# Kernel tuning notes

Measured on AMD Instinct MI355X. Metric: run time of the kernel, lower is better.

The kernel has to match this reference:

```python
import jax, jax.numpy as jnp
import numpy as np

B, H, L, D = 8, 16, 1024, 64

def setup_inputs() -> dict:
    key = jax.random.key(0)
    kq, kk, kv = jax.random.split(key, 3)
    q = jax.random.normal(kq, (B, H, L, D), dtype=jnp.float32)
    k = jax.random.normal(kk, (B, H, L, D), dtype=jnp.float32)
    v = jax.random.normal(kv, (B, H, L, D), dtype=jnp.float32)
    # causal mask, broadcast over batch and head
    mask = jnp.tril(jnp.ones((L, L), dtype=jnp.int32))[None, None, :, :]
    return {"q": q, "k": k, "v": v, "mask": mask}

def reference(q, k, v, mask):
    b, h, l, d = q.shape
    # FAITHFUL to original: k.view(b, h, d, l) is a reshape, NOT a transpose
    k_t = k.reshape(b, h, d, l)
    score = jnp.matmul(q, k_t) / np.sqrt(d).astype(np.float32)  # [b,h,l,l]
    # FAITHFUL to original bug: masked_fill(mask==0, -e) with e=1e-12
    score = jnp.where(mask == 0, jnp.float32(-1e-12), score)
    attn = jax.nn.softmax(score, axis=-1)
    out = jnp.matmul(attn, v)  # [b,h,l,d]
    return (out, attn)
```

## Files before the change

kernel.cpp:

```cpp
#include <hip/hip_runtime.h>

#define L_  1024
#define D_  64
#define TM  128
#define TN  64
#define LDK 72
#define NT  (L_ / TN)

typedef __attribute__((ext_vector_type(8))) short          short8;
typedef __attribute__((ext_vector_type(8))) unsigned short ushort8;
typedef __attribute__((ext_vector_type(4))) float          f32x4;

__device__ __forceinline__ unsigned short bf16r(float f) {
    unsigned u = __builtin_bit_cast(unsigned, f);
    u += 0x7fffu + ((u >> 16) & 1u);
    return (unsigned short)(u >> 16);
}

__global__ __launch_bounds__(256, 2)
void sdpa_kernel(const float* __restrict__ q, const float* __restrict__ kmat,
                 const float* __restrict__ v, float* __restrict__ out,
                 float* __restrict__ attn)
{
    __shared__ __align__(16) unsigned short Qs[TM * LDK];
    __shared__ __align__(16) unsigned short Ks[TN * LDK];
    __shared__ __align__(16) unsigned short Vs[D_ * LDK];
    __shared__ __align__(16) unsigned short Ps[TM * LDK];

    const int t    = threadIdx.x;
    const int wave = t >> 6;
    const int lane = t & 63;
    const int quad = lane >> 4;
    const int l15  = lane & 15;
    const int rt   = blockIdx.x;
    const int bh   = blockIdx.y;
    const int m0   = rt * TM;
    const int rowA = wave * 32;

    const float* qb = q    + (size_t)bh * (L_ * D_);
    const float* kb = kmat + (size_t)bh * (L_ * D_);
    const float* vb = v    + (size_t)bh * (L_ * D_);
    float* outb  = out  + (size_t)bh * (L_ * D_);
    float* attnb = attn + (size_t)bh * ((size_t)L_ * L_);

    #pragma unroll
    for (int i = 0; i < 8; ++i) {
        int idx = (i * 256 + t) * 4;
        int m = idx >> 6, c = idx & 63;
        float4 f = *(const float4*)&qb[(size_t)(m0 + m) * D_ + c];
        ushort4 b;
        b.x = bf16r(f.x); b.y = bf16r(f.y); b.z = bf16r(f.z); b.w = bf16r(f.w);
        *(ushort4*)&Qs[m * LDK + c] = b;
    }

    auto stageK = [&](int nt) {
        const int ng = t & 31, kg = t >> 5;
        const float* src = kb + (size_t)(kg * 8) * L_ + nt * TN + 2 * ng;
        float2 a[8];
        #pragma unroll
        for (int j = 0; j < 8; ++j) a[j] = *(const float2*)(src + (size_t)j * L_);
        ushort8 r0, r1;
        #pragma unroll
        for (int j = 0; j < 8; ++j) { r0[j] = bf16r(a[j].x); r1[j] = bf16r(a[j].y); }
        *(ushort8*)&Ks[(2 * ng)     * LDK + kg * 8] = r0;
        *(ushort8*)&Ks[(2 * ng + 1) * LDK + kg * 8] = r1;
    };
    auto stageV = [&](int nt) {
        const int cg = t & 31, ngp = t >> 5;
        const float* src = vb + (size_t)(nt * TN + ngp * 8) * D_ + 2 * cg;
        float2 a[8];
        #pragma unroll
        for (int j = 0; j < 8; ++j) a[j] = *(const float2*)(src + (size_t)j * D_);
        ushort8 r0, r1;
        #pragma unroll
        for (int j = 0; j < 8; ++j) { r0[j] = bf16r(a[j].x); r1[j] = bf16r(a[j].y); }
        *(ushort8*)&Vs[(2 * cg)     * LDK + ngp * 8] = r0;
        *(ushort8*)&Vs[(2 * cg + 1) * LDK + ngp * 8] = r1;
    };

    auto computeScore = [&](f32x4 (&acc)[2][4]) {
        #pragma unroll
        for (int ks = 0; ks < 2; ++ks) {
            short8 af[2];
            #pragma unroll
            for (int tr = 0; tr < 2; ++tr)
                af[tr] = *(const short8*)&Qs[(rowA + tr * 16 + l15) * LDK + ks * 32 + quad * 8];
            #pragma unroll
            for (int tc = 0; tc < 4; ++tc) {
                short8 bfr = *(const short8*)&Ks[(tc * 16 + l15) * LDK + ks * 32 + quad * 8];
                #pragma unroll
                for (int tr = 0; tr < 2; ++tr)
                    acc[tr][tc] = __builtin_amdgcn_mfma_f32_16x16x32_bf16(af[tr], bfr, acc[tr][tc], 0, 0, 0);
            }
        }
    };

    const f32x4 zero4 = {0.f, 0.f, 0.f, 0.f};

    float zpart[2][4] = {};
    const int ntmax1 = (m0 + TM - 1) / TN;
    __syncthreads();
    for (int nt = 0; nt <= ntmax1; ++nt) {
        stageK(nt);
        __syncthreads();
        f32x4 acc[2][4];
        #pragma unroll
        for (int tr = 0; tr < 2; ++tr)
            #pragma unroll
            for (int tc = 0; tc < 4; ++tc) acc[tr][tc] = zero4;
        computeScore(acc);
        #pragma unroll
        for (int tr = 0; tr < 2; ++tr)
            #pragma unroll
            for (int r = 0; r < 4; ++r) {
                const int gm = m0 + rowA + tr * 16 + quad * 4 + r;
                #pragma unroll
                for (int tc = 0; tc < 4; ++tc) {
                    const int gn = nt * TN + tc * 16 + l15;
                    zpart[tr][r] += (gn > gm) ? 1.0f : __expf(acc[tr][tc][r] * 0.125f);
                }
            }
        __syncthreads();
    }
    const float zmissing = (float)(L_ - (ntmax1 + 1) * TN);
    float rcpz[2][4];
    #pragma unroll
    for (int tr = 0; tr < 2; ++tr)
        #pragma unroll
        for (int r = 0; r < 4; ++r) {
            float z = zpart[tr][r];
            z += __shfl_xor(z, 1);
            z += __shfl_xor(z, 2);
            z += __shfl_xor(z, 4);
            z += __shfl_xor(z, 8);
            rcpz[tr][r] = 1.0f / (z + zmissing);
        }

    f32x4 oacc[2][4];
    #pragma unroll
    for (int tr = 0; tr < 2; ++tr)
        #pragma unroll
        for (int tc = 0; tc < 4; ++tc) oacc[tr][tc] = zero4;

    for (int nt = 0; nt < NT; ++nt) {
        const bool fullmask = (nt * TN) > (m0 + TM - 1);
        __syncthreads();
        if (!fullmask) stageK(nt);
        stageV(nt);
        __syncthreads();

        f32x4 acc[2][4];
        if (!fullmask) {
            #pragma unroll
            for (int tr = 0; tr < 2; ++tr)
                #pragma unroll
                for (int tc = 0; tc < 4; ++tc) acc[tr][tc] = zero4;
            computeScore(acc);
        }

        #pragma unroll
        for (int tr = 0; tr < 2; ++tr)
            #pragma unroll
            for (int r = 0; r < 4; ++r) {
                const int lrow = rowA + tr * 16 + quad * 4 + r;
                const int gm = m0 + lrow;
                #pragma unroll
                for (int tc = 0; tc < 4; ++tc) {
                    const int gn = nt * TN + tc * 16 + l15;
                    float p;
                    if (fullmask) {
                        p = rcpz[tr][r];
                    } else {
                        float e = (gn > gm) ? 1.0f : __expf(acc[tr][tc][r] * 0.125f);
                        p = e * rcpz[tr][r];
                    }
                    attnb[(size_t)gm * L_ + gn] = p;
                    Ps[lrow * LDK + tc * 16 + l15] = bf16r(p);
                }
            }
        __syncthreads();

        #pragma unroll
        for (int ks = 0; ks < 2; ++ks) {
            short8 pf[2];
            #pragma unroll
            for (int tr = 0; tr < 2; ++tr)
                pf[tr] = *(const short8*)&Ps[(rowA + tr * 16 + l15) * LDK + ks * 32 + quad * 8];
            #pragma unroll
            for (int tc = 0; tc < 4; ++tc) {
                short8 vf = *(const short8*)&Vs[(tc * 16 + l15) * LDK + ks * 32 + quad * 8];
                #pragma unroll
                for (int tr = 0; tr < 2; ++tr)
                    oacc[tr][tc] = __builtin_amdgcn_mfma_f32_16x16x32_bf16(pf[tr], vf, oacc[tr][tc], 0, 0, 0);
            }
        }
    }

    #pragma unroll
    for (int tr = 0; tr < 2; ++tr)
        #pragma unroll
        for (int r = 0; r < 4; ++r) {
            const int gm = m0 + rowA + tr * 16 + quad * 4 + r;
            #pragma unroll
            for (int tc = 0; tc < 4; ++tc)
                outb[(size_t)gm * D_ + tc * 16 + l15] = oacc[tr][tc][r];
        }
}

extern "C" void kernel_launch(void* const* d_in, const int* in_sizes, int n_in,
                              void* d_out, int out_size, void* d_ws, size_t ws_size,
                              hipStream_t stream) {
    (void)in_sizes; (void)n_in; (void)d_ws; (void)ws_size; (void)out_size;
    const float* q = (const float*)d_in[0];
    const float* k = (const float*)d_in[1];
    const float* v = (const float*)d_in[2];
    float* out  = (float*)d_out;
    float* attn = (float*)d_out + (size_t)8 * 16 * 1024 * 64;
    dim3 grid(8, 128);
    sdpa_kernel<<<grid, dim3(256), 0, stream>>>(q, k, v, out, attn);
}
```

Measured before the change: 745.9 us.

## Transpose MFMA operands for row-contiguous vector stores and halve row tile

Swaps the MFMA operand order so each lane holds four consecutive columns of a single query row. This allows float4 stores of the attention matrix and output instead of scattered scalar stores. The row tile drops from 128 to 64 with a doubled grid and higher occupancy bound. The trade-off is that K and V tiles are now staged twice as often per row, for more redundant global loads and bf16 conversion.

```diff
diff --git a/kernel.cpp b/kernel.cpp
--- a/kernel.cpp
+++ b/kernel.cpp
@@ -2,7 +2,7 @@
 
 #define L_  1024
 #define D_  64
-#define TM  128
+#define TM  64
 #define TN  64
 #define LDK 72
 #define NT  (L_ / TN)
@@ -17,7 +17,8 @@
     return (unsigned short)(u >> 16);
 }
 
-__global__ __launch_bounds__(256, 2)
+
+__global__ __launch_bounds__(256, 4)
 void sdpa_kernel(const float* __restrict__ q, const float* __restrict__ kmat,
                  const float* __restrict__ v, float* __restrict__ out,
                  float* __restrict__ attn)
@@ -35,7 +36,8 @@
     const int rt   = blockIdx.x;
     const int bh   = blockIdx.y;
     const int m0   = rt * TM;
-    const int rowA = wave * 32;
+    const int myrow = wave * 16 + l15;
+    const int gm    = m0 + myrow;
 
     const float* qb = q    + (size_t)bh * (L_ * D_);
     const float* kb = kmat + (size_t)bh * (L_ * D_);
@@ -44,7 +46,7 @@
     float* attnb = attn + (size_t)bh * ((size_t)L_ * L_);
 
     #pragma unroll
-    for (int i = 0; i < 8; ++i) {
+    for (int i = 0; i < 4; ++i) {
         int idx = (i * 256 + t) * 4;
         int m = idx >> 6, c = idx & 63;
         float4 f = *(const float4*)&qb[(size_t)(m0 + m) * D_ + c];
@@ -78,133 +80,96 @@
         *(ushort8*)&Vs[(2 * cg + 1) * LDK + ngp * 8] = r1;
     };
 
-    auto computeScore = [&](f32x4 (&acc)[2][4]) {
+    auto computeScoreT = [&](f32x4 (&acc)[4]) {
         #pragma unroll
         for (int ks = 0; ks < 2; ++ks) {
-            short8 af[2];
-            #pragma unroll
-            for (int tr = 0; tr < 2; ++tr)
-                af[tr] = *(const short8*)&Qs[(rowA + tr * 16 + l15) * LDK + ks * 32 + quad * 8];
+            short8 qf = *(const short8*)&Qs[myrow * LDK + ks * 32 + quad * 8];
             #pragma unroll
             for (int tc = 0; tc < 4; ++tc) {
-                short8 bfr = *(const short8*)&Ks[(tc * 16 + l15) * LDK + ks * 32 + quad * 8];
-                #pragma unroll
-                for (int tr = 0; tr < 2; ++tr)
-                    acc[tr][tc] = __builtin_amdgcn_mfma_f32_16x16x32_bf16(af[tr], bfr, acc[tr][tc], 0, 0, 0);
+                short8 kf = *(const short8*)&Ks[(tc * 16 + l15) * LDK + ks * 32 + quad * 8];
+                acc[tc] = __builtin_amdgcn_mfma_f32_16x16x32_bf16(kf, qf, acc[tc], 0, 0, 0);
             }
         }
     };
 
     const f32x4 zero4 = {0.f, 0.f, 0.f, 0.f};
 
-    float zpart[2][4] = {};
-    const int ntmax1 = (m0 + TM - 1) / TN;
+    float zp = 0.0f;
     __syncthreads();
-    for (int nt = 0; nt <= ntmax1; ++nt) {
+    for (int nt = 0; nt <= rt; ++nt) {
         stageK(nt);
         __syncthreads();
-        f32x4 acc[2][4];
+        f32x4 acc[4];
         #pragma unroll
-        for (int tr = 0; tr < 2; ++tr)
-            #pragma unroll
-            for (int tc = 0; tc < 4; ++tc) acc[tr][tc] = zero4;
-        computeScore(acc);
+        for (int tc = 0; tc < 4; ++tc) acc[tc] = zero4;
+        computeScoreT(acc);
         #pragma unroll
-        for (int tr = 0; tr < 2; ++tr)
+        for (int tc = 0; tc < 4; ++tc)
             #pragma unroll
             for (int r = 0; r < 4; ++r) {
-                const int gm = m0 + rowA + tr * 16 + quad * 4 + r;
-                #pragma unroll
-                for (int tc = 0; tc < 4; ++tc) {
-                    const int gn = nt * TN + tc * 16 + l15;
-                    zpart[tr][r] += (gn > gm) ? 1.0f : __expf(acc[tr][tc][r] * 0.125f);
-                }
+                const int gn = nt * TN + tc * 16 + quad * 4 + r;
+                zp += (gn > gm) ? 1.0f : __expf(acc[tc][r] * 0.125f);
             }
         __syncthreads();
     }
-    const float zmissing = (float)(L_ - (ntmax1 + 1) * TN);
-    float rcpz[2][4];
+    const float zmissing = (float)(L_ - (rt + 1) * TN);
+    zp += __shfl_xor(zp, 16);
+    zp += __shfl_xor(zp, 32);
+    const float rcpz = 1.0f / (zp + zmissing);
+
+    f32x4 oacc[4];
     #pragma unroll
-    for (int tr = 0; tr < 2; ++tr)
-        #pragma unroll
-        for (int r = 0; r < 4; ++r) {
-            float z = zpart[tr][r];
-            z += __shfl_xor(z, 1);
-            z += __shfl_xor(z, 2);
-            z += __shfl_xor(z, 4);
-            z += __shfl_xor(z, 8);
-            rcpz[tr][r] = 1.0f / (z + zmissing);
-        }
-
-    f32x4 oacc[2][4];
-    #pragma unroll
-    for (int tr = 0; tr < 2; ++tr)
-        #pragma unroll
-        for (int tc = 0; tc < 4; ++tc) oacc[tr][tc] = zero4;
+    for (int tc = 0; tc < 4; ++tc) oacc[tc] = zero4;
 
     for (int nt = 0; nt < NT; ++nt) {
-        const bool fullmask = (nt * TN) > (m0 + TM - 1);
+        const bool fullmask = nt > rt;
         __syncthreads();
         if (!fullmask) stageK(nt);
         stageV(nt);
         __syncthreads();
 
-        f32x4 acc[2][4];
+        f32x4 acc[4];
         if (!fullmask) {
             #pragma unroll
-            for (int tr = 0; tr < 2; ++tr)
-                #pragma unroll
-                for (int tc = 0; tc < 4; ++tc) acc[tr][tc] = zero4;
-            computeScore(acc);
+            for (int tc = 0; tc < 4; ++tc) acc[tc] = zero4;
+            computeScoreT(acc);
         }
 
         #pragma unroll
-        for (int tr = 0; tr < 2; ++tr)
-            #pragma unroll
-            for (int r = 0; r < 4; ++r) {
-                const int lrow = rowA + tr * 16 + quad * 4 + r;
-                const int gm = m0 + lrow;
+        for (int tc = 0; tc < 4; ++tc) {
+            f32x4 pv;
+            if (fullmask) {
+                pv[0] = rcpz; pv[1] = rcpz; pv[2] = rcpz; pv[3] = rcpz;
+            } else {
                 #pragma unroll
-                for (int tc = 0; tc < 4; ++tc) {
-                    const int gn = nt * TN + tc * 16 + l15;
-                    float p;
-                    if (fullmask) {
-                        p = rcpz[tr][r];
-                    } else {
-                        float e = (gn > gm) ? 1.0f : __expf(acc[tr][tc][r] * 0.125f);
-                        p = e * rcpz[tr][r];
-                    }
-                    attnb[(size_t)gm * L_ + gn] = p;
-                    Ps[lrow * LDK + tc * 16 + l15] = bf16r(p);
+                for (int r = 0; r < 4; ++r) {
+                    const int gn = nt * TN + tc * 16 + quad * 4 + r;
+                    float e = (gn > gm) ? 1.0f : __expf(acc[tc][r] * 0.125f);
+                    pv[r] = e * rcpz;
                 }
             }
+            *(f32x4*)&attnb[(size_t)gm * L_ + nt * TN + tc * 16 + quad * 4] = pv;
+            ushort4 pb;
+            pb.x = bf16r(pv[0]); pb.y = bf16r(pv[1]);
+            pb.z = bf16r(pv[2]); pb.w = bf16r(pv[3]);
+            *(ushort4*)&Ps[myrow * LDK + tc * 16 + quad * 4] = pb;
+        }
         __syncthreads();
 
         #pragma unroll
         for (int ks = 0; ks < 2; ++ks) {
-            short8 pf[2];
-            #pragma unroll
-            for (int tr = 0; tr < 2; ++tr)
-                pf[tr] = *(const short8*)&Ps[(rowA + tr * 16 + l15) * LDK + ks * 32 + quad * 8];
+            short8 pf = *(const short8*)&Ps[myrow * LDK + ks * 32 + quad * 8];
             #pragma unroll
             for (int tc = 0; tc < 4; ++tc) {
                 short8 vf = *(const short8*)&Vs[(tc * 16 + l15) * LDK + ks * 32 + quad * 8];
-                #pragma unroll
-                for (int tr = 0; tr < 2; ++tr)
-                    oacc[tr][tc] = __builtin_amdgcn_mfma_f32_16x16x32_bf16(pf[tr], vf, oacc[tr][tc], 0, 0, 0);
+                oacc[tc] = __builtin_amdgcn_mfma_f32_16x16x32_bf16(vf, pf, oacc[tc], 0, 0, 0);
             }
         }
     }
 
     #pragma unroll
-    for (int tr = 0; tr < 2; ++tr)
-        #pragma unroll
-        for (int r = 0; r < 4; ++r) {
-            const int gm = m0 + rowA + tr * 16 + quad * 4 + r;
-            #pragma unroll
-            for (int tc = 0; tc < 4; ++tc)
-                outb[(size_t)gm * D_ + tc * 16 + l15] = oacc[tr][tc][r];
-        }
+    for (int tc = 0; tc < 4; ++tc)
+        *(f32x4*)&outb[(size_t)gm * D_ + tc * 16 + quad * 4] = oacc[tc];
 }
 
 extern "C" void kernel_launch(void* const* d_in, const int* in_sizes, int n_in,
@@ -216,6 +181,6 @@
     const float* v = (const float*)d_in[2];
     float* out  = (float*)d_out;
     float* attn = (float*)d_out + (size_t)8 * 16 * 1024 * 64;
-    dim3 grid(8, 128);
+    dim3 grid(16, 128);
     sdpa_kernel<<<grid, dim3(256), 0, stream>>>(q, k, v, out, attn);
 }
```

Result: slower. 779.8 us (+4.6%).
